# Kernel optimization log

Hardware: AMD Instinct MI355X
Metric: run time of the kernel (lower is better)

Reference implementation:

```python
import jax, jax.numpy as jnp
import numpy as np

jax.config.update("jax_enable_x64", True)  # exact int64 fixed-point requantization

QMIN, QMAX = 0, 255  # 8-bit asymmetric activations


def _mul_m0_shift(acc, M0, shift):
    """gemmlowp-style fixed-point rescale: round((acc*M0)>>31) >> shift (rounding)."""
    prod = acc.astype(jnp.int64) * M0.astype(jnp.int64)
    nudge = jnp.where(prod >= 0, jnp.int64(1 << 30), jnp.int64(1 - (1 << 30)))
    hi = (prod + nudge) >> 31  # rounding-doubling high mul
    sh = shift.astype(jnp.int64)
    return (hi + (jnp.int64(1) << (sh - 1))) >> sh  # rounding right shift


def _requant(acc, M0, shift, z_out):
    return jnp.clip(_mul_m0_shift(acc, M0, shift) + z_out, QMIN, QMAX).astype(jnp.int32)


def _qconv(q, w, z_in, M0, shift, z_out, pad):
    # int8-style conv: subtract input zero-point, integer accumulate (exact in fp32
    # since |acc| < 2^24 by construction), then fixed-point requantize.
    xf = (q - z_in).astype(jnp.float32)
    acc = jax.lax.conv_general_dilated(
        xf, w, (1, 1), [(pad, pad), (pad, pad)],
        dimension_numbers=("NCHW", "OIHW", "NCHW"))
    return _requant(jnp.round(acc).astype(jnp.int64), M0, shift, z_out)


def _qbn(q, z_in, w, b, M0, shift, z_out):
    # fused quantized BN: per-channel integer affine + fixed-point requantize
    acc = (q.astype(jnp.int64) - z_in) * w.astype(jnp.int64)[None, :, None, None] \
          + b.astype(jnp.int64)[None, :, None, None]
    return _requant(acc, M0, shift, z_out)


def setup_inputs() -> dict:
    key = jax.random.key(0)
    ks = jax.random.split(key, 10)
    B, Cin, H, W = 32, 256, 56, 56
    width, Cout = 64, 256
    x = jax.random.randint(ks[0], (B, Cin, H, W), 0, 256, dtype=jnp.int32)
    w1 = jax.random.randint(ks[1], (width, Cin, 1, 1), -63, 64).astype(jnp.float32)
    w2 = jax.random.randint(ks[2], (width, width, 3, 3), -63, 64).astype(jnp.float32)
    w3 = jax.random.randint(ks[3], (Cout, width, 1, 1), -63, 64).astype(jnp.float32)
    bn1_w = jax.random.randint(ks[4], (width,), 100, 160).astype(jnp.float32)
    bn1_b = jax.random.randint(ks[5], (width,), -1000, 1000).astype(jnp.float32)
    bn2_w = jax.random.randint(ks[6], (width,), 100, 160).astype(jnp.float32)
    bn2_b = jax.random.randint(ks[7], (width,), -1000, 1000).astype(jnp.float32)
    bn3_w = jax.random.randint(ks[8], (Cout,), 100, 160).astype(jnp.float32)
    bn3_b = jax.random.randint(ks[9], (Cout,), -1000, 1000).astype(jnp.float32)
    conv_zin = jnp.array([128, 128, 128], jnp.int32)
    conv_m0 = jnp.array([1518500250] * 3, jnp.int32)
    conv_shift = jnp.array([9, 9, 9], jnp.int32)
    conv_zout = jnp.array([128, 128, 128], jnp.int32)
    bn_m0 = jnp.array([1073741824] * 3, jnp.int32)
    bn_shift = jnp.array([6, 6, 6], jnp.int32)
    bn_zout = jnp.array([128, 128, 128], jnp.int32)
    add_z = jnp.array([128, 128], jnp.int32)
    add_m0 = jnp.array([1073741824] * 2, jnp.int32)
    add_shift = jnp.array([1, 1], jnp.int32)
    add_zout = jnp.array(128, jnp.int32)
    return dict(x=x, w1=w1, w2=w2, w3=w3,
                bn1_w=bn1_w, bn1_b=bn1_b, bn2_w=bn2_w, bn2_b=bn2_b,
                bn3_w=bn3_w, bn3_b=bn3_b,
                conv_zin=conv_zin, conv_m0=conv_m0, conv_shift=conv_shift,
                conv_zout=conv_zout, bn_m0=bn_m0, bn_shift=bn_shift,
                bn_zout=bn_zout, add_z=add_z, add_m0=add_m0,
                add_shift=add_shift, add_zout=add_zout)


def reference(x, w1, w2, w3, bn1_w, bn1_b, bn2_w, bn2_b, bn3_w, bn3_b,
              conv_zin, conv_m0, conv_shift, conv_zout,
              bn_m0, bn_shift, bn_zout,
              add_z, add_m0, add_shift, add_zout):
    identity = x  # a_bit == target_bit -> rescale_matrix path skipped, conv_x = x
    out = _qconv(x, w1, conv_zin[0], conv_m0[0], conv_shift[0], conv_zout[0], 0)
    out = _qbn(out, conv_zout[0], bn1_w, bn1_b, bn_m0[0], bn_shift[0], bn_zout[0])
    out = _qconv(out, w2, conv_zin[1], conv_m0[1], conv_shift[1], conv_zout[1], 1)
    out = _qbn(out, conv_zout[1], bn2_w, bn2_b, bn_m0[1], bn_shift[1], bn_zout[1])
    out = _qconv(out, w3, conv_zin[2], conv_m0[2], conv_shift[2], conv_zout[2], 0)
    out = _qbn(out, conv_zout[2], bn3_w, bn3_b, bn_m0[2], bn_shift[2], bn_zout[2])
    # QuantizedAdd: rescale both branches to the output scale, add, clamp
    ra = _mul_m0_shift(identity.astype(jnp.int64) - add_z[0], add_m0[0], add_shift[0])
    rb = _mul_m0_shift(out.astype(jnp.int64) - add_z[1], add_m0[1], add_shift[1])
    return jnp.clip(ra + rb + add_zout, QMIN, QMAX).astype(jnp.int32)
```

## Files before the change

### kernel.cpp

```cpp
#include <hip/hip_runtime.h>


typedef int v4i __attribute__((ext_vector_type(4)));

#define BATCH 32
#define CIN 256
#define CMID 64
#define HW 3136
#define W56 56

#define T1_BYTES ((size_t)BATCH * HW * CMID)
#define WP_BYTES ((size_t)68 * 64 * 16)

__device__ __forceinline__ int requant_f(int acc, int M0, long long pAdd,
                                         long long nAdd, int tSh, int zout) {
    long long prod = (long long)acc * (long long)M0;
    long long add = (prod >= 0) ? pAdd : nAdd;
    int v = (int)((prod + add) >> tSh) + zout;
    return v < 0 ? 0 : (v > 255 ? 255 : v);
}

__device__ __forceinline__ v4i pack16f(const float* src, int stride) {
    v4i r;
#pragma unroll
    for (int d = 0; d < 4; ++d) {
        unsigned int u = 0;
#pragma unroll
        for (int by = 0; by < 4; ++by) {
            int v = (int)src[(d * 4 + by) * stride];
            u |= ((unsigned int)(v & 255)) << (8 * by);
        }
        r[d] = (int)u;
    }
    return r;
}

__global__ __launch_bounds__(256) void k_prep(
    const float* __restrict__ w1, const float* __restrict__ w2,
    const float* __restrict__ w3, v4i* __restrict__ wp)
{
    int id = blockIdx.x * 256 + threadIdx.x;
    int fid = id >> 6, lane = id & 63;
    if (fid >= 68) return;
    int col = lane & 15, ci0 = (lane >> 4) * 16;
    const float* src;
    int stride;
    if (fid < 16) {
        int wv = fid >> 2, ks = fid & 3;
        src = w1 + (size_t)(wv * 16 + col) * 256 + ks * 64 + ci0;
        stride = 1;
    } else if (fid < 52) {
        int i = fid - 16, wv = i / 9, t = i - wv * 9;
        src = w2 + ((size_t)(wv * 16 + col) * 64 + ci0) * 9 + t;
        stride = 9;
    } else {
        int s = fid - 52;
        src = w3 + (size_t)(s * 16 + col) * 64 + ci0;
        stride = 1;
    }
    wp[fid * 64 + lane] = pack16f(src, stride);
}

__global__ __launch_bounds__(256, 4) void k_conv1(
    const int* __restrict__ x, const v4i* __restrict__ wp1,
    const float* __restrict__ bn_w, const float* __restrict__ bn_b,
    const int* __restrict__ conv_zin, const int* __restrict__ conv_m0,
    const int* __restrict__ conv_shift, const int* __restrict__ conv_zout,
    const int* __restrict__ bn_m0, const int* __restrict__ bn_shift,
    const int* __restrict__ bn_zout, signed char* __restrict__ t1)
{
    __shared__ v4i sm[560];
    const int tid = threadIdx.x, lane = tid & 63, wv = tid >> 6;
    const int col = lane & 15, koff = lane >> 4;
    const int b = blockIdx.y;
    const int hw0 = blockIdx.x * 112;
    const int co0 = wv * 16;

    v4i a[4];
#pragma unroll
    for (int ks = 0; ks < 4; ++ks) a[ks] = wp1[(wv * 4 + ks) * 64 + lane];

    const int cg = tid & 7, q = tid >> 3;
    const bool act = q < 28;
    const int zin = conv_zin[0];
    const int* xbase = x + (size_t)b * CIN * HW + hw0 + 4 * q;

    v4i xa[8], xa2[8];
    if (act) {
#pragma unroll
        for (int j = 0; j < 8; ++j)
            xa[j] = *(const v4i*)(xbase + (size_t)(cg * 8 + j) * HW);
    }

    v4i acc[7];
#pragma unroll
    for (int i = 0; i < 7; ++i) acc[i] = (v4i){0, 0, 0, 0};

    unsigned long long* smu = (unsigned long long*)sm;
#pragma unroll
    for (int ks = 0; ks < 4; ++ks) {
        if (ks) __syncthreads();
        if (act) {
#pragma unroll
            for (int p = 0; p < 4; ++p) {
                unsigned int lo = 0, hi = 0;
#pragma unroll
                for (int j = 0; j < 4; ++j) {
                    lo |= ((unsigned int)((xa[j][p] - zin) & 255)) << (8 * j);
                    hi |= ((unsigned int)((xa[j + 4][p] - zin) & 255)) << (8 * j);
                }
                smu[(q * 4 + p) * 10 + cg] = ((unsigned long long)hi << 32) | lo;
            }
        }
        __syncthreads();
        if (ks < 3 && act) {
#pragma unroll
            for (int j = 0; j < 8; ++j)
                xa2[j] = *(const v4i*)(xbase + (size_t)((ks + 1) * 64 + cg * 8 + j) * HW);
        }
#pragma unroll
        for (int nt = 0; nt < 7; ++nt) {
            v4i bf = sm[(nt * 16 + col) * 5 + koff];
            acc[nt] = __builtin_amdgcn_mfma_i32_16x16x64_i8(a[ks], bf, acc[nt], 0, 0, 0);
        }
        if (ks < 3) {
#pragma unroll
            for (int j = 0; j < 8; ++j) xa[j] = xa2[j];
        }
    }

    const int cm0 = conv_m0[0], csh = conv_shift[0], czo = conv_zout[0];
    const int bm0 = bn_m0[0], bsh = bn_shift[0], bzo = bn_zout[0];
    const long long cP = (1LL << 30) + (1LL << (30 + csh));
    const long long cN = (1LL - (1LL << 30)) + (1LL << (30 + csh));
    const long long bP = (1LL << 30) + (1LL << (30 + bsh));
    const long long bN = (1LL - (1LL << 30)) + (1LL << (30 + bsh));
    const int cT = 31 + csh, bT = 31 + bsh;
    const int zin2 = conv_zin[1];
    const int rowb = koff * 4;
    int bw[4], bb[4];
#pragma unroll
    for (int r = 0; r < 4; ++r) {
        bw[r] = (int)bn_w[co0 + rowb + r];
        bb[r] = (int)bn_b[co0 + rowb + r];
    }
#pragma unroll
    for (int nt = 0; nt < 7; ++nt) {
        int n = b * HW + hw0 + nt * 16 + col;
        unsigned int pkd = 0;
#pragma unroll
        for (int r = 0; r < 4; ++r) {
            int qv = requant_f(acc[nt][r], cm0, cP, cN, cT, czo);
            int a2 = (qv - czo) * bw[r] + bb[r];
            int q2 = requant_f(a2, bm0, bP, bN, bT, bzo);
            pkd |= ((unsigned int)((q2 - zin2) & 255)) << (8 * r);
        }
        *(unsigned int*)(t1 + (size_t)n * 64 + co0 + rowb) = pkd;
    }
}

__global__ __launch_bounds__(256, 4) void k_conv2(
    const signed char* __restrict__ t1, const v4i* __restrict__ wp2,
    const float* __restrict__ bn_w, const float* __restrict__ bn_b,
    const int* __restrict__ conv_zin, const int* __restrict__ conv_m0,
    const int* __restrict__ conv_shift, const int* __restrict__ conv_zout,
    const int* __restrict__ bn_m0, const int* __restrict__ bn_shift,
    const int* __restrict__ bn_zout, signed char* __restrict__ t2)
{
    __shared__ v4i sm[1740];
    const int tid = threadIdx.x, lane = tid & 63, wv = tid >> 6;
    const int col = lane & 15, koff = lane >> 4;
    const int b = blockIdx.y;
    const int r0 = blockIdx.x * 4;
    const int co0 = wv * 16;

    v4i a[9];
#pragma unroll
    for (int t = 0; t < 9; ++t) a[t] = wp2[(wv * 9 + t) * 64 + lane];

    const v4i* t1v = (const v4i*)t1;
#pragma unroll
    for (int k = 0; k < 6; ++k) {
        int idx = tid + k * 256;
        if (idx < 1344) {
            int pixl = idx >> 2, part = idx & 3;
            int lrow = pixl / W56, gw = pixl - lrow * W56;
            int grow = r0 - 1 + lrow;
            v4i v = (v4i){0, 0, 0, 0};
            if ((unsigned)grow < 56u)
                v = t1v[((size_t)b * HW + grow * W56 + gw) * 4 + part];
            sm[(lrow * 58 + gw + 1) * 5 + part] = v;
        }
    }
    if (tid < 48) {
        int e = tid >> 2, part = tid & 3;
        int row = e >> 1, side = e & 1;
        sm[(row * 58 + side * 57) * 5 + part] = (v4i){0, 0, 0, 0};
    }
    __syncthreads();

    int basep[14];
#pragma unroll
    for (int nt = 0; nt < 14; ++nt) {
        int pix = nt * 16 + col;
        int orow = pix / W56, wc = pix - orow * W56;
        basep[nt] = (orow * 58 + wc) * 5 + koff;
    }

    v4i acc[14];
#pragma unroll
    for (int i = 0; i < 14; ++i) acc[i] = (v4i){0, 0, 0, 0};

#pragma unroll
    for (int kh = 0; kh < 3; ++kh) {
#pragma unroll
        for (int kw = 0; kw < 3; ++kw) {
            v4i af = a[kh * 3 + kw];
            const int toff = (kh * 58 + kw) * 5;
#pragma unroll
            for (int nt = 0; nt < 14; ++nt) {
                v4i bf = sm[basep[nt] + toff];
                acc[nt] = __builtin_amdgcn_mfma_i32_16x16x64_i8(af, bf, acc[nt], 0, 0, 0);
            }
        }
    }

    const int cm0 = conv_m0[1], csh = conv_shift[1], czo = conv_zout[1];
    const int bm0 = bn_m0[1], bsh = bn_shift[1], bzo = bn_zout[1];
    const long long cP = (1LL << 30) + (1LL << (30 + csh));
    const long long cN = (1LL - (1LL << 30)) + (1LL << (30 + csh));
    const long long bP = (1LL << 30) + (1LL << (30 + bsh));
    const long long bN = (1LL - (1LL << 30)) + (1LL << (30 + bsh));
    const int cT = 31 + csh, bT = 31 + bsh;
    const int zin3 = conv_zin[2];
    const int rowb = koff * 4;
    int bw[4], bb[4];
#pragma unroll
    for (int r = 0; r < 4; ++r) {
        bw[r] = (int)bn_w[co0 + rowb + r];
        bb[r] = (int)bn_b[co0 + rowb + r];
    }
#pragma unroll
    for (int nt = 0; nt < 14; ++nt) {
        int pix = nt * 16 + col;
        int n = b * HW + r0 * W56 + pix;
        unsigned int pkd = 0;
#pragma unroll
        for (int r = 0; r < 4; ++r) {
            int qv = requant_f(acc[nt][r], cm0, cP, cN, cT, czo);
            int a2 = (qv - czo) * bw[r] + bb[r];
            int q2 = requant_f(a2, bm0, bP, bN, bT, bzo);
            pkd |= ((unsigned int)((q2 - zin3) & 255)) << (8 * r);
        }
        *(unsigned int*)(t2 + (size_t)n * 64 + co0 + rowb) = pkd;
    }
}

__global__ __launch_bounds__(256, 4) void k_conv3(
    const signed char* __restrict__ t2, const v4i* __restrict__ wp3,
    const float* __restrict__ bn_w, const float* __restrict__ bn_b,
    const int* __restrict__ x,
    const int* __restrict__ conv_m0, const int* __restrict__ conv_shift,
    const int* __restrict__ conv_zout,
    const int* __restrict__ bn_m0, const int* __restrict__ bn_shift,
    const int* __restrict__ bn_zout,
    const int* __restrict__ add_z, const int* __restrict__ add_m0,
    const int* __restrict__ add_shift, const int* __restrict__ add_zout,
    int* __restrict__ out)
{
    __shared__ v4i sm[640];
    __shared__ int lutA[256], lutB[256];
    const int tid = threadIdx.x, lane = tid & 63, wv = tid >> 6;
    const int col = lane & 15, koff = lane >> 4;
    const int nbase = blockIdx.x * 128;
    const int co0 = blockIdx.y * 64 + wv * 16;
    const int rowb = koff * 4;

    v4i a = wp3[(blockIdx.y * 4 + wv) * 64 + lane];

    {
        const int az0 = add_z[0], az1 = add_z[1];
        const int am0 = add_m0[0], am1 = add_m0[1];
        const int ash0 = add_shift[0], ash1 = add_shift[1];
        const int azout = add_zout[0];
        long long pA = (long long)(tid - az0) * am0;
        long long pB = (long long)(tid - az1) * am1;
        long long P0 = (1LL << 30) + (1LL << (30 + ash0));
        long long N0 = (1LL - (1LL << 30)) + (1LL << (30 + ash0));
        long long P1 = (1LL << 30) + (1LL << (30 + ash1));
        long long N1 = (1LL - (1LL << 30)) + (1LL << (30 + ash1));
        lutA[tid] = (int)((pA + (pA >= 0 ? P0 : N0)) >> (31 + ash0));
        lutB[tid] = (int)((pB + (pB >= 0 ? P1 : N1)) >> (31 + ash1)) + azout;
    }

    int nn[8], pb[8], phw[8];
#pragma unroll
    for (int nt = 0; nt < 8; ++nt) {
        nn[nt] = nbase + nt * 16 + col;
        pb[nt] = nn[nt] / HW;
        phw[nt] = nn[nt] - pb[nt] * HW;
    }
    int xv[8][4];
#pragma unroll
    for (int nt = 0; nt < 8; ++nt)
#pragma unroll
        for (int r = 0; r < 4; ++r)
            xv[nt][r] = x[((size_t)pb[nt] * CIN + co0 + rowb + r) * HW + phw[nt]];

    const v4i* t2v = (const v4i*)t2;
#pragma unroll
    for (int k = 0; k < 2; ++k) {
        int idx = tid + k * 256;
        int pixl = idx >> 2, part = idx & 3;
        sm[pixl * 5 + part] = t2v[(size_t)(nbase + pixl) * 4 + part];
    }
    __syncthreads();

    v4i acc[8];
#pragma unroll
    for (int i = 0; i < 8; ++i) acc[i] = (v4i){0, 0, 0, 0};
#pragma unroll
    for (int nt = 0; nt < 8; ++nt) {
        v4i bf = sm[(nt * 16 + col) * 5 + koff];
        acc[nt] = __builtin_amdgcn_mfma_i32_16x16x64_i8(a, bf, acc[nt], 0, 0, 0);
    }

    const int cm0 = conv_m0[2], csh = conv_shift[2], czo = conv_zout[2];
    const int bm0 = bn_m0[2], bsh = bn_shift[2], bzo = bn_zout[2];
    const long long cP = (1LL << 30) + (1LL << (30 + csh));
    const long long cN = (1LL - (1LL << 30)) + (1LL << (30 + csh));
    const long long bP = (1LL << 30) + (1LL << (30 + bsh));
    const long long bN = (1LL - (1LL << 30)) + (1LL << (30 + bsh));
    const int cT = 31 + csh, bT = 31 + bsh;
    int bw[4], bb[4];
#pragma unroll
    for (int r = 0; r < 4; ++r) {
        bw[r] = (int)bn_w[co0 + rowb + r];
        bb[r] = (int)bn_b[co0 + rowb + r];
    }
#pragma unroll
    for (int nt = 0; nt < 8; ++nt) {
#pragma unroll
        for (int r = 0; r < 4; ++r) {
            int qv = requant_f(acc[nt][r], cm0, cP, cN, cT, czo);
            int a2 = (qv - czo) * bw[r] + bb[r];
            int q2 = requant_f(a2, bm0, bP, bN, bT, bzo);
            int res = lutA[xv[nt][r]] + lutB[q2];
            res = res < 0 ? 0 : (res > 255 ? 255 : res);
            out[((size_t)pb[nt] * CIN + co0 + rowb + r) * HW + phw[nt]] = res;
        }
    }
}

extern "C" void kernel_launch(void* const* d_in, const int* in_sizes, int n_in,
                              void* d_out, int out_size, void* d_ws, size_t ws_size,
                              hipStream_t stream) {
    const int* x = (const int*)d_in[0];
    const float* w1 = (const float*)d_in[1];
    const float* w2 = (const float*)d_in[2];
    const float* w3 = (const float*)d_in[3];
    const float* bn1_w = (const float*)d_in[4];
    const float* bn1_b = (const float*)d_in[5];
    const float* bn2_w = (const float*)d_in[6];
    const float* bn2_b = (const float*)d_in[7];
    const float* bn3_w = (const float*)d_in[8];
    const float* bn3_b = (const float*)d_in[9];
    const int* conv_zin = (const int*)d_in[10];
    const int* conv_m0 = (const int*)d_in[11];
    const int* conv_shift = (const int*)d_in[12];
    const int* conv_zout = (const int*)d_in[13];
    const int* bn_m0 = (const int*)d_in[14];
    const int* bn_shift = (const int*)d_in[15];
    const int* bn_zout = (const int*)d_in[16];
    const int* add_z = (const int*)d_in[17];
    const int* add_m0 = (const int*)d_in[18];
    const int* add_shift = (const int*)d_in[19];
    const int* add_zout = (const int*)d_in[20];

    v4i* wp = (v4i*)d_ws;
    signed char* t1 = (signed char*)d_ws + WP_BYTES;
    signed char* t2 = t1 + T1_BYTES;

    const v4i* wp1 = wp;
    const v4i* wp2 = wp + 16 * 64;
    const v4i* wp3 = wp + 52 * 64;

    k_prep<<<dim3(17), dim3(256), 0, stream>>>(w1, w2, w3, wp);
    k_conv1<<<dim3(28, 32), dim3(256), 0, stream>>>(x, wp1, bn1_w, bn1_b,
        conv_zin, conv_m0, conv_shift, conv_zout, bn_m0, bn_shift, bn_zout, t1);
    k_conv2<<<dim3(14, 32), dim3(256), 0, stream>>>(t1, wp2, bn2_w, bn2_b,
        conv_zin, conv_m0, conv_shift, conv_zout, bn_m0, bn_shift, bn_zout, t2);
    k_conv3<<<dim3(784, 4), dim3(256), 0, stream>>>(t2, wp3, bn3_w, bn3_b,
        x, conv_m0, conv_shift, conv_zout, bn_m0, bn_shift, bn_zout,
        add_z, add_m0, add_shift, add_zout, (int*)d_out);
}
```

Before: 283.7 us.

## Fuse three bottleneck conv stages into one kernel with halo recompute

Replaces the three separate conv kernels with a single kernel per (batch, 4-row strip). Each block computes conv1 on six rows (including halo rows), keeps the intermediate in shared memory, runs the 3x3 conv2 from there, then conv3 with the residual add. This removes the global round trips for the t1 and t2 intermediates and two kernel launches. In exchange it recomputes conv1 on halo rows (about 1.5x conv1 work), uses more shared memory and registers (launch bounds drop to 2 blocks per SU), and launches only 448 blocks, which lowers occupancy.

```diff
diff --git a/kernel.cpp b/kernel.cpp
--- a/kernel.cpp
+++ b/kernel.cpp
@@ -8,8 +8,6 @@
 #define CMID 64
 #define HW 3136
 #define W56 56
-
-#define T1_BYTES ((size_t)BATCH * HW * CMID)
 #define WP_BYTES ((size_t)68 * 64 * 16)
 
 __device__ __forceinline__ int requant_f(int acc, int M0, long long pAdd,
@@ -61,222 +59,28 @@
     wp[fid * 64 + lane] = pack16f(src, stride);
 }
 
-__global__ __launch_bounds__(256, 4) void k_conv1(
-    const int* __restrict__ x, const v4i* __restrict__ wp1,
-    const float* __restrict__ bn_w, const float* __restrict__ bn_b,
+__global__ __launch_bounds__(256, 2) void k_fused(
+    const int* __restrict__ x, const v4i* __restrict__ wp,
+    const float* __restrict__ bn1_w, const float* __restrict__ bn1_b,
+    const float* __restrict__ bn2_w, const float* __restrict__ bn2_b,
+    const float* __restrict__ bn3_w, const float* __restrict__ bn3_b,
     const int* __restrict__ conv_zin, const int* __restrict__ conv_m0,
     const int* __restrict__ conv_shift, const int* __restrict__ conv_zout,
-    const int* __restrict__ bn_m0, const int* __restrict__ bn_shift,
-    const int* __restrict__ bn_zout, signed char* __restrict__ t1)
-{
-    __shared__ v4i sm[560];
-    const int tid = threadIdx.x, lane = tid & 63, wv = tid >> 6;
-    const int col = lane & 15, koff = lane >> 4;
-    const int b = blockIdx.y;
-    const int hw0 = blockIdx.x * 112;
-    const int co0 = wv * 16;
-
-    v4i a[4];
-#pragma unroll
-    for (int ks = 0; ks < 4; ++ks) a[ks] = wp1[(wv * 4 + ks) * 64 + lane];
-
-    const int cg = tid & 7, q = tid >> 3;
-    const bool act = q < 28;
-    const int zin = conv_zin[0];
-    const int* xbase = x + (size_t)b * CIN * HW + hw0 + 4 * q;
-
-    v4i xa[8], xa2[8];
-    if (act) {
-#pragma unroll
-        for (int j = 0; j < 8; ++j)
-            xa[j] = *(const v4i*)(xbase + (size_t)(cg * 8 + j) * HW);
-    }
-
-    v4i acc[7];
-#pragma unroll
-    for (int i = 0; i < 7; ++i) acc[i] = (v4i){0, 0, 0, 0};
-
-    unsigned long long* smu = (unsigned long long*)sm;
-#pragma unroll
-    for (int ks = 0; ks < 4; ++ks) {
-        if (ks) __syncthreads();
-        if (act) {
-#pragma unroll
-            for (int p = 0; p < 4; ++p) {
-                unsigned int lo = 0, hi = 0;
-#pragma unroll
-                for (int j = 0; j < 4; ++j) {
-                    lo |= ((unsigned int)((xa[j][p] - zin) & 255)) << (8 * j);
-                    hi |= ((unsigned int)((xa[j + 4][p] - zin) & 255)) << (8 * j);
-                }
-                smu[(q * 4 + p) * 10 + cg] = ((unsigned long long)hi << 32) | lo;
-            }
-        }
-        __syncthreads();
-        if (ks < 3 && act) {
-#pragma unroll
-            for (int j = 0; j < 8; ++j)
-                xa2[j] = *(const v4i*)(xbase + (size_t)((ks + 1) * 64 + cg * 8 + j) * HW);
-        }
-#pragma unroll
-        for (int nt = 0; nt < 7; ++nt) {
-            v4i bf = sm[(nt * 16 + col) * 5 + koff];
-            acc[nt] = __builtin_amdgcn_mfma_i32_16x16x64_i8(a[ks], bf, acc[nt], 0, 0, 0);
-        }
-        if (ks < 3) {
-#pragma unroll
-            for (int j = 0; j < 8; ++j) xa[j] = xa2[j];
-        }
-    }
-
-    const int cm0 = conv_m0[0], csh = conv_shift[0], czo = conv_zout[0];
-    const int bm0 = bn_m0[0], bsh = bn_shift[0], bzo = bn_zout[0];
-    const long long cP = (1LL << 30) + (1LL << (30 + csh));
-    const long long cN = (1LL - (1LL << 30)) + (1LL << (30 + csh));
-    const long long bP = (1LL << 30) + (1LL << (30 + bsh));
-    const long long bN = (1LL - (1LL << 30)) + (1LL << (30 + bsh));
-    const int cT = 31 + csh, bT = 31 + bsh;
-    const int zin2 = conv_zin[1];
-    const int rowb = koff * 4;
-    int bw[4], bb[4];
-#pragma unroll
-    for (int r = 0; r < 4; ++r) {
-        bw[r] = (int)bn_w[co0 + rowb + r];
-        bb[r] = (int)bn_b[co0 + rowb + r];
-    }
-#pragma unroll
-    for (int nt = 0; nt < 7; ++nt) {
-        int n = b * HW + hw0 + nt * 16 + col;
-        unsigned int pkd = 0;
-#pragma unroll
-        for (int r = 0; r < 4; ++r) {
-            int qv = requant_f(acc[nt][r], cm0, cP, cN, cT, czo);
-            int a2 = (qv - czo) * bw[r] + bb[r];
-            int q2 = requant_f(a2, bm0, bP, bN, bT, bzo);
-            pkd |= ((unsigned int)((q2 - zin2) & 255)) << (8 * r);
-        }
-        *(unsigned int*)(t1 + (size_t)n * 64 + co0 + rowb) = pkd;
-    }
-}
-
-__global__ __launch_bounds__(256, 4) void k_conv2(
-    const signed char* __restrict__ t1, const v4i* __restrict__ wp2,
-    const float* __restrict__ bn_w, const float* __restrict__ bn_b,
-    const int* __restrict__ conv_zin, const int* __restrict__ conv_m0,
-    const int* __restrict__ conv_shift, const int* __restrict__ conv_zout,
-    const int* __restrict__ bn_m0, const int* __restrict__ bn_shift,
-    const int* __restrict__ bn_zout, signed char* __restrict__ t2)
-{
-    __shared__ v4i sm[1740];
-    const int tid = threadIdx.x, lane = tid & 63, wv = tid >> 6;
-    const int col = lane & 15, koff = lane >> 4;
-    const int b = blockIdx.y;
-    const int r0 = blockIdx.x * 4;
-    const int co0 = wv * 16;
-
-    v4i a[9];
-#pragma unroll
-    for (int t = 0; t < 9; ++t) a[t] = wp2[(wv * 9 + t) * 64 + lane];
-
-    const v4i* t1v = (const v4i*)t1;
-#pragma unroll
-    for (int k = 0; k < 6; ++k) {
-        int idx = tid + k * 256;
-        if (idx < 1344) {
-            int pixl = idx >> 2, part = idx & 3;
-            int lrow = pixl / W56, gw = pixl - lrow * W56;
-            int grow = r0 - 1 + lrow;
-            v4i v = (v4i){0, 0, 0, 0};
-            if ((unsigned)grow < 56u)
-                v = t1v[((size_t)b * HW + grow * W56 + gw) * 4 + part];
-            sm[(lrow * 58 + gw + 1) * 5 + part] = v;
-        }
-    }
-    if (tid < 48) {
-        int e = tid >> 2, part = tid & 3;
-        int row = e >> 1, side = e & 1;
-        sm[(row * 58 + side * 57) * 5 + part] = (v4i){0, 0, 0, 0};
-    }
-    __syncthreads();
-
-    int basep[14];
-#pragma unroll
-    for (int nt = 0; nt < 14; ++nt) {
-        int pix = nt * 16 + col;
-        int orow = pix / W56, wc = pix - orow * W56;
-        basep[nt] = (orow * 58 + wc) * 5 + koff;
-    }
-
-    v4i acc[14];
-#pragma unroll
-    for (int i = 0; i < 14; ++i) acc[i] = (v4i){0, 0, 0, 0};
-
-#pragma unroll
-    for (int kh = 0; kh < 3; ++kh) {
-#pragma unroll
-        for (int kw = 0; kw < 3; ++kw) {
-            v4i af = a[kh * 3 + kw];
-            const int toff = (kh * 58 + kw) * 5;
-#pragma unroll
-            for (int nt = 0; nt < 14; ++nt) {
-                v4i bf = sm[basep[nt] + toff];
-                acc[nt] = __builtin_amdgcn_mfma_i32_16x16x64_i8(af, bf, acc[nt], 0, 0, 0);
-            }
-        }
-    }
-
-    const int cm0 = conv_m0[1], csh = conv_shift[1], czo = conv_zout[1];
-    const int bm0 = bn_m0[1], bsh = bn_shift[1], bzo = bn_zout[1];
-    const long long cP = (1LL << 30) + (1LL << (30 + csh));
-    const long long cN = (1LL - (1LL << 30)) + (1LL << (30 + csh));
-    const long long bP = (1LL << 30) + (1LL << (30 + bsh));
-    const long long bN = (1LL - (1LL << 30)) + (1LL << (30 + bsh));
-    const int cT = 31 + csh, bT = 31 + bsh;
-    const int zin3 = conv_zin[2];
-    const int rowb = koff * 4;
-    int bw[4], bb[4];
-#pragma unroll
-    for (int r = 0; r < 4; ++r) {
-        bw[r] = (int)bn_w[co0 + rowb + r];
-        bb[r] = (int)bn_b[co0 + rowb + r];
-    }
-#pragma unroll
-    for (int nt = 0; nt < 14; ++nt) {
-        int pix = nt * 16 + col;
-        int n = b * HW + r0 * W56 + pix;
-        unsigned int pkd = 0;
-#pragma unroll
-        for (int r = 0; r < 4; ++r) {
-            int qv = requant_f(acc[nt][r], cm0, cP, cN, cT, czo);
-            int a2 = (qv - czo) * bw[r] + bb[r];
-            int q2 = requant_f(a2, bm0, bP, bN, bT, bzo);
-            pkd |= ((unsigned int)((q2 - zin3) & 255)) << (8 * r);
-        }
-        *(unsigned int*)(t2 + (size_t)n * 64 + co0 + rowb) = pkd;
-    }
-}
-
-__global__ __launch_bounds__(256, 4) void k_conv3(
-    const signed char* __restrict__ t2, const v4i* __restrict__ wp3,
-    const float* __restrict__ bn_w, const float* __restrict__ bn_b,
-    const int* __restrict__ x,
-    const int* __restrict__ conv_m0, const int* __restrict__ conv_shift,
-    const int* __restrict__ conv_zout,
     const int* __restrict__ bn_m0, const int* __restrict__ bn_shift,
     const int* __restrict__ bn_zout,
     const int* __restrict__ add_z, const int* __restrict__ add_m0,
     const int* __restrict__ add_shift, const int* __restrict__ add_zout,
     int* __restrict__ out)
 {
-    __shared__ v4i sm[640];
+    __shared__ v4i smX[1680];
+    __shared__ v4i smM[1740];
     __shared__ int lutA[256], lutB[256];
+
     const int tid = threadIdx.x, lane = tid & 63, wv = tid >> 6;
     const int col = lane & 15, koff = lane >> 4;
-    const int nbase = blockIdx.x * 128;
-    const int co0 = blockIdx.y * 64 + wv * 16;
+    const int b = blockIdx.y, r0 = blockIdx.x * 4;
     const int rowb = koff * 4;
-
-    v4i a = wp3[(blockIdx.y * 4 + wv) * 64 + lane];
+    const int co0 = wv * 16;
 
     {
         const int az0 = add_z[0], az1 = add_z[1];
@@ -292,62 +96,218 @@
         lutA[tid] = (int)((pA + (pA >= 0 ? P0 : N0)) >> (31 + ash0));
         lutB[tid] = (int)((pB + (pB >= 0 ? P1 : N1)) >> (31 + ash1)) + azout;
     }
-
-    int nn[8], pb[8], phw[8];
-#pragma unroll
-    for (int nt = 0; nt < 8; ++nt) {
-        nn[nt] = nbase + nt * 16 + col;
-        pb[nt] = nn[nt] / HW;
-        phw[nt] = nn[nt] - pb[nt] * HW;
-    }
-    int xv[8][4];
-#pragma unroll
-    for (int nt = 0; nt < 8; ++nt)
+    if (tid < 192) {
+        int e = tid >> 4, d = tid & 15;
+        int row = e >> 1, side = e & 1;
+        ((int*)smM)[(row * 58 + side * 57) * 20 + d] = 0;
+    }
+
+    const int zin = conv_zin[0];
+    v4i a1[4];
+#pragma unroll
+    for (int ks = 0; ks < 4; ++ks) a1[ks] = wp[(wv * 4 + ks) * 64 + lane];
+
+    v4i accA[21];
+#pragma unroll
+    for (int i = 0; i < 21; ++i) accA[i] = (v4i){0, 0, 0, 0};
+
+    unsigned long long* smuX = (unsigned long long*)smX;
+    for (int ks = 0; ks < 4; ++ks) {
+        if (ks) __syncthreads();
+#pragma unroll
+        for (int u = 0; u < 3; ++u) {
+            int unit = tid + u * 256;
+            if (unit < 672) {
+                int cg = unit & 7, qq = unit >> 3;
+                int row = qq / 14, quad = qq - row * 14;
+                int grow = r0 - 1 + row;
+                v4i xa[8];
+                if ((unsigned)grow < 56u) {
+                    const int* xb = x + (size_t)(b * CIN + ks * 64 + cg * 8) * HW
+                                      + grow * W56 + quad * 4;
+#pragma unroll
+                    for (int j = 0; j < 8; ++j)
+                        xa[j] = *(const v4i*)(xb + (size_t)j * HW);
+                } else {
+#pragma unroll
+                    for (int j = 0; j < 8; ++j) {
+                        v4i z; z[0] = zin; z[1] = zin; z[2] = zin; z[3] = zin;
+                        xa[j] = z;
+                    }
+                }
+#pragma unroll
+                for (int p = 0; p < 4; ++p) {
+                    unsigned int lo = 0, hi = 0;
+#pragma unroll
+                    for (int j = 0; j < 4; ++j) {
+                        lo |= ((unsigned int)((xa[j][p] - zin) & 255)) << (8 * j);
+                        hi |= ((unsigned int)((xa[j + 4][p] - zin) & 255)) << (8 * j);
+                    }
+                    smuX[(qq * 4 + p) * 10 + cg] = ((unsigned long long)hi << 32) | lo;
+                }
+            }
+        }
+        __syncthreads();
+#pragma unroll
+        for (int nt = 0; nt < 21; ++nt) {
+            v4i bf = smX[(nt * 16 + col) * 5 + koff];
+            accA[nt] = __builtin_amdgcn_mfma_i32_16x16x64_i8(a1[ks], bf, accA[nt], 0, 0, 0);
+        }
+    }
+
+    {
+        const int cm0 = conv_m0[0], csh = conv_shift[0], czo = conv_zout[0];
+        const int bm0 = bn_m0[0], bsh = bn_shift[0], bzo = bn_zout[0];
+        const long long cP = (1LL << 30) + (1LL << (30 + csh));
+        const long long cN = (1LL - (1LL << 30)) + (1LL << (30 + csh));
+        const long long bP = (1LL << 30) + (1LL << (30 + bsh));
+        const long long bN = (1LL - (1LL << 30)) + (1LL << (30 + bsh));
+        const int cT = 31 + csh, bT = 31 + bsh;
+        const int zin2 = conv_zin[1];
+        int bw[4], bb[4];
+#pragma unroll
+        for (int r = 0; r < 4; ++r) {
+            bw[r] = (int)bn1_w[co0 + rowb + r];
+            bb[r] = (int)bn1_b[co0 + rowb + r];
+        }
+#pragma unroll
+        for (int nt = 0; nt < 21; ++nt) {
+            int px = nt * 16 + col;
+            int row = px / W56, gw = px - row * W56;
+            int grow = r0 - 1 + row;
+            unsigned int pkd = 0;
+            if ((unsigned)grow < 56u) {
+#pragma unroll
+                for (int r = 0; r < 4; ++r) {
+                    int q1 = requant_f(accA[nt][r], cm0, cP, cN, cT, czo);
+                    int a2 = (q1 - czo) * bw[r] + bb[r];
+                    int q2 = requant_f(a2, bm0, bP, bN, bT, bzo);
+                    pkd |= ((unsigned int)((q2 - zin2) & 255)) << (8 * r);
+                }
+            }
+            ((int*)smM)[(row * 58 + 1 + gw) * 20 + wv * 4 + koff] = (int)pkd;
+        }
+    }
+    __syncthreads();
+
+    v4i a2f[9];
+#pragma unroll
+    for (int t = 0; t < 9; ++t) a2f[t] = wp[(16 + wv * 9 + t) * 64 + lane];
+
+    int basep[14];
+#pragma unroll
+    for (int nt = 0; nt < 14; ++nt) {
+        int pix = nt * 16 + col;
+        int orow = pix / W56, wc = pix - orow * W56;
+        basep[nt] = (orow * 58 + wc) * 5 + koff;
+    }
+
+    v4i accB[14];
+#pragma unroll
+    for (int i = 0; i < 14; ++i) accB[i] = (v4i){0, 0, 0, 0};
+#pragma unroll
+    for (int kh = 0; kh < 3; ++kh) {
+#pragma unroll
+        for (int kw = 0; kw < 3; ++kw) {
+            v4i af = a2f[kh * 3 + kw];
+            const int toff = (kh * 58 + kw) * 5;
+#pragma unroll
+            for (int nt = 0; nt < 14; ++nt) {
+                v4i bf = smM[basep[nt] + toff];
+                accB[nt] = __builtin_amdgcn_mfma_i32_16x16x64_i8(af, bf, accB[nt], 0, 0, 0);
+            }
+        }
+    }
+
+    {
+        const int cm0 = conv_m0[1], csh = conv_shift[1], czo = conv_zout[1];
+        const int bm0 = bn_m0[1], bsh = bn_shift[1], bzo = bn_zout[1];
+        const long long cP = (1LL << 30) + (1LL << (30 + csh));
+        const long long cN = (1LL - (1LL << 30)) + (1LL << (30 + csh));
+        const long long bP = (1LL << 30) + (1LL << (30 + bsh));
+        const long long bN = (1LL - (1LL << 30)) + (1LL << (30 + bsh));
+        const int cT = 31 + csh, bT = 31 + bsh;
+        const int zin3 = conv_zin[2];
+        int bw[4], bb[4];
+#pragma unroll
+        for (int r = 0; r < 4; ++r) {
+            bw[r] = (int)bn2_w[co0 + rowb + r];
+            bb[r] = (int)bn2_b[co0 + rowb + r];
+        }
+#pragma unroll
+        for (int nt = 0; nt < 14; ++nt) {
+            unsigned int pkd = 0;
+#pragma unroll
+            for (int r = 0; r < 4; ++r) {
+                int q1 = requant_f(accB[nt][r], cm0, cP, cN, cT, czo);
+                int a2 = (q1 - czo) * bw[r] + bb[r];
+                int q2 = requant_f(a2, bm0, bP, bN, bT, bzo);
+                pkd |= ((unsigned int)((q2 - zin3) & 255)) << (8 * r);
+            }
+            ((int*)smX)[(nt * 16 + col) * 20 + wv * 4 + koff] = (int)pkd;
+        }
+    }
+
+    v4i a3f[4];
+#pragma unroll
+    for (int f = 0; f < 4; ++f) a3f[f] = wp[(52 + wv * 4 + f) * 64 + lane];
+    const int ghw0 = r0 * W56;
+    int xcur[4][4], xnxt[4][4];
+#pragma unroll
+    for (int f = 0; f < 4; ++f)
 #pragma unroll
         for (int r = 0; r < 4; ++r)
-            xv[nt][r] = x[((size_t)pb[nt] * CIN + co0 + rowb + r) * HW + phw[nt]];
-
-    const v4i* t2v = (const v4i*)t2;
-#pragma unroll
-    for (int k = 0; k < 2; ++k) {
-        int idx = tid + k * 256;
-        int pixl = idx >> 2, part = idx & 3;
-        sm[pixl * 5 + part] = t2v[(size_t)(nbase + pixl) * 4 + part];
-    }
+            xcur[f][r] = x[(size_t)(b * CIN + wv * 64 + f * 16 + rowb + r) * HW + ghw0 + col];
     __syncthreads();
 
-    v4i acc[8];
-#pragma unroll
-    for (int i = 0; i < 8; ++i) acc[i] = (v4i){0, 0, 0, 0};
-#pragma unroll
-    for (int nt = 0; nt < 8; ++nt) {
-        v4i bf = sm[(nt * 16 + col) * 5 + koff];
-        acc[nt] = __builtin_amdgcn_mfma_i32_16x16x64_i8(a, bf, acc[nt], 0, 0, 0);
-    }
-
-    const int cm0 = conv_m0[2], csh = conv_shift[2], czo = conv_zout[2];
-    const int bm0 = bn_m0[2], bsh = bn_shift[2], bzo = bn_zout[2];
-    const long long cP = (1LL << 30) + (1LL << (30 + csh));
-    const long long cN = (1LL - (1LL << 30)) + (1LL << (30 + csh));
-    const long long bP = (1LL << 30) + (1LL << (30 + bsh));
-    const long long bN = (1LL - (1LL << 30)) + (1LL << (30 + bsh));
-    const int cT = 31 + csh, bT = 31 + bsh;
-    int bw[4], bb[4];
-#pragma unroll
-    for (int r = 0; r < 4; ++r) {
-        bw[r] = (int)bn_w[co0 + rowb + r];
-        bb[r] = (int)bn_b[co0 + rowb + r];
-    }
-#pragma unroll
-    for (int nt = 0; nt < 8; ++nt) {
-#pragma unroll
-        for (int r = 0; r < 4; ++r) {
-            int qv = requant_f(acc[nt][r], cm0, cP, cN, cT, czo);
-            int a2 = (qv - czo) * bw[r] + bb[r];
-            int q2 = requant_f(a2, bm0, bP, bN, bT, bzo);
-            int res = lutA[xv[nt][r]] + lutB[q2];
-            res = res < 0 ? 0 : (res > 255 ? 255 : res);
-            out[((size_t)pb[nt] * CIN + co0 + rowb + r) * HW + phw[nt]] = res;
+    {
+        const int cm0 = conv_m0[2], csh = conv_shift[2], czo = conv_zout[2];
+        const int bm0 = bn_m0[2], bsh = bn_shift[2], bzo = bn_zout[2];
+        const long long cP = (1LL << 30) + (1LL << (30 + csh));
+        const long long cN = (1LL - (1LL << 30)) + (1LL << (30 + csh));
+        const long long bP = (1LL << 30) + (1LL << (30 + bsh));
+        const long long bN = (1LL - (1LL << 30)) + (1LL << (30 + bsh));
+        const int cT = 31 + csh, bT = 31 + bsh;
+        int bw[4][4], bb[4][4];
+#pragma unroll
+        for (int f = 0; f < 4; ++f)
+#pragma unroll
+            for (int r = 0; r < 4; ++r) {
+                bw[f][r] = (int)bn3_w[wv * 64 + f * 16 + rowb + r];
+                bb[f][r] = (int)bn3_b[wv * 64 + f * 16 + rowb + r];
+            }
+        const v4i zf = (v4i){0, 0, 0, 0};
+#pragma unroll
+        for (int nt = 0; nt < 14; ++nt) {
+            if (nt < 13) {
+#pragma unroll
+                for (int f = 0; f < 4; ++f)
+#pragma unroll
+                    for (int r = 0; r < 4; ++r)
+                        xnxt[f][r] = x[(size_t)(b * CIN + wv * 64 + f * 16 + rowb + r) * HW
+                                       + ghw0 + (nt + 1) * 16 + col];
+            }
+            v4i bf = smX[(nt * 16 + col) * 5 + koff];
+            v4i accC[4];
+#pragma unroll
+            for (int f = 0; f < 4; ++f)
+                accC[f] = __builtin_amdgcn_mfma_i32_16x16x64_i8(a3f[f], bf, zf, 0, 0, 0);
+#pragma unroll
+            for (int f = 0; f < 4; ++f)
+#pragma unroll
+                for (int r = 0; r < 4; ++r) {
+                    int q1 = requant_f(accC[f][r], cm0, cP, cN, cT, czo);
+                    int a2 = (q1 - czo) * bw[f][r] + bb[f][r];
+                    int q2 = requant_f(a2, bm0, bP, bN, bT, bzo);
+                    int res = lutA[xcur[f][r]] + lutB[q2];
+                    res = res < 0 ? 0 : (res > 255 ? 255 : res);
+                    out[(size_t)(b * CIN + wv * 64 + f * 16 + rowb + r) * HW
+                        + ghw0 + nt * 16 + col] = res;
+                }
+#pragma unroll
+            for (int f = 0; f < 4; ++f)
+#pragma unroll
+                for (int r = 0; r < 4; ++r) xcur[f][r] = xnxt[f][r];
         }
     }
 }
@@ -378,19 +338,10 @@
     const int* add_zout = (const int*)d_in[20];
 
     v4i* wp = (v4i*)d_ws;
-    signed char* t1 = (signed char*)d_ws + WP_BYTES;
-    signed char* t2 = t1 + T1_BYTES;
-
-    const v4i* wp1 = wp;
-    const v4i* wp2 = wp + 16 * 64;
-    const v4i* wp3 = wp + 52 * 64;
 
     k_prep<<<dim3(17), dim3(256), 0, stream>>>(w1, w2, w3, wp);
-    k_conv1<<<dim3(28, 32), dim3(256), 0, stream>>>(x, wp1, bn1_w, bn1_b,
-        conv_zin, conv_m0, conv_shift, conv_zout, bn_m0, bn_shift, bn_zout, t1);
-    k_conv2<<<dim3(14, 32), dim3(256), 0, stream>>>(t1, wp2, bn2_w, bn2_b,
-        conv_zin, conv_m0, conv_shift, conv_zout, bn_m0, bn_shift, bn_zout, t2);
-    k_conv3<<<dim3(784, 4), dim3(256), 0, stream>>>(t2, wp3, bn3_w, bn3_b,
-        x, conv_m0, conv_shift, conv_zout, bn_m0, bn_shift, bn_zout,
+    k_fused<<<dim3(14, 32), dim3(256), 0, stream>>>(x, wp,
+        bn1_w, bn1_b, bn2_w, bn2_b, bn3_w, bn3_b,
+        conv_zin, conv_m0, conv_shift, conv_zout, bn_m0, bn_shift, bn_zout,
         add_z, add_m0, add_shift, add_zout, (int*)d_out);
 }
```

Result: no change. 281.5 us (-0.8%).
